# Optimization experiments

Hardware: AMD Instinct MI355X
Metric: run time of the kernel (lower is better)

The kernel has to match this reference:

```python
import jax, jax.numpy as jnp
import numpy as np
from jax import lax

B, T, S = 32, 64, 400
H, E, EMB, V = 512, 1024, 256, 32000


def setup_inputs() -> dict:
    key = jax.random.key(0)
    ks = jax.random.split(key, 16)
    w = lambda k, shape: jax.random.normal(k, shape, dtype=jnp.float32) * 0.05
    return {
        "target": jax.random.randint(ks[0], (B, T), 0, V),
        "h0": jax.random.normal(ks[1], (B, H), dtype=jnp.float32),
        "c0": jax.random.normal(ks[2], (B, H), dtype=jnp.float32),
        "enc_outs": jax.random.normal(ks[3], (S, B, E), dtype=jnp.float32),
        "attn_mask": jnp.ones((B, S), dtype=jnp.int32),
        "emb": w(ks[4], (V, EMB)),
        "W_ih": w(ks[5], (4 * H, EMB)),
        "b_ih": w(ks[6], (4 * H,)),
        "W_hh": w(ks[7], (4 * H, H)),
        "b_hh": w(ks[8], (4 * H,)),
        "W_attn": w(ks[9], (H, E)),
        "b_attn": w(ks[10], (H,)),
        "W_concat": w(ks[11], (H, E + H)),
        "b_concat": w(ks[12], (H,)),
        "W_out": w(ks[13], (V, H)),
        "b_out": w(ks[14], (V,)),
    }


def reference(target, h0, c0, enc_outs, attn_mask, emb, W_ih, b_ih, W_hh, b_hh,
              W_attn, b_attn, W_concat, b_concat, W_out, b_out):
    # Precompute attention keys projection once: [S, B, H]
    keys_proj = jnp.einsum("sbe,he->sbh", enc_outs, W_attn) + b_attn
    masked = attn_mask == 0  # [B, S]
    x_seq = emb[target].transpose(1, 0, 2)  # [T, B, EMB]

    def step(carry, x_t):
        h, c = carry
        # LSTMCell (torch gate order: i, f, g, o)
        gates = x_t @ W_ih.T + b_ih + h @ W_hh.T + b_hh  # [B, 4H]
        i, f, g, o = jnp.split(gates, 4, axis=1)
        c = jax.nn.sigmoid(f) * c + jax.nn.sigmoid(i) * jnp.tanh(g)
        h = jax.nn.sigmoid(o) * jnp.tanh(c)
        # additive-style attention: sum over hidden of query*key_proj
        scores = jnp.einsum("bh,sbh->bs", h, keys_proj)  # [B, S]
        scores = jnp.where(masked, jnp.float32(-1e18), scores)
        a = jax.nn.softmax(scores, axis=1)
        ctx = jnp.einsum("bs,sbe->be", a, enc_outs)  # [B, E]
        cat = jnp.tanh(jnp.concatenate([ctx, h], axis=1) @ W_concat.T + b_concat)
        logit = jax.nn.log_softmax(cat @ W_out.T + b_out, axis=-1)  # [B, V]
        return (h, c), logit

    (_, _), logits = lax.scan(step, (h0, c0), x_seq)  # [T, B, V]
    return logits.transpose(1, 0, 2)  # [B, T, V]
```

## Files before the change

### kernel.cpp

```cpp
#include <hip/hip_runtime.h>
#include <hip/hip_bf16.h>
#include <hip/hip_fp16.h>

#define B_ 32
#define T_ 64
#define S_ 400
#define H_ 512
#define E_ 1024
#define EMB_ 256
#define V_ 32000

typedef _Float16 f16;
typedef _Float16 half8 __attribute__((ext_vector_type(8)));
typedef float f32x4 __attribute__((ext_vector_type(4)));
typedef float f32x16 __attribute__((ext_vector_type(16)));
typedef unsigned uint4v __attribute__((ext_vector_type(4)));

__device__ __forceinline__ void gl_lds16(const void* g, void* l) {
  __builtin_amdgcn_global_load_lds(
      (const __attribute__((address_space(1))) void*)g,
      (__attribute__((address_space(3))) void*)l, 16, 0, 0);
}

__device__ __forceinline__ float sigmoidf_(float x) { return 1.f / (1.f + expf(-x)); }

__device__ __forceinline__ uint4v load_b128_sys(const void* p) {
  uint4v r;
  asm volatile("global_load_dwordx4 %0, %1, off sc0 sc1" : "=v"(r) : "v"(p) : "memory");
  return r;
}
__device__ __forceinline__ void store_b128_sys(void* p, uint4v v) {
  asm volatile("global_store_dwordx4 %0, %1, off sc0 sc1" :: "v"(p), "v"(v) : "memory");
}

__global__ __launch_bounds__(256) void cvt_f16_kernel(const float* __restrict__ src,
                                                      f16* __restrict__ dst, int n2) {
  int i = blockIdx.x * 256 + threadIdx.x;
  if (i >= n2) return;
  float2 v = reinterpret_cast<const float2*>(src)[i];
  union { f16 h[2]; unsigned u; } o;
  o.h[0] = (f16)v.x; o.h[1] = (f16)v.y;
  reinterpret_cast<unsigned*>(dst)[i] = o.u;
}

__global__ __launch_bounds__(256) void gather_x_kernel(const int* __restrict__ target,
                                                       const float* __restrict__ emb,
                                                       f16* __restrict__ xin) {
  int r = blockIdx.x;
  int t = r >> 5, b = r & 31;
  int tok = target[b * T_ + t];
  xin[(size_t)r * EMB_ + threadIdx.x] = (f16)emb[(size_t)tok * EMB_ + threadIdx.x];
}

__global__ __launch_bounds__(256) void prep_kernel(const float* __restrict__ b_ih,
                                                   const float* __restrict__ b_hh,
                                                   float* __restrict__ biasperm,
                                                   const float* __restrict__ Whh,
                                                   f16* __restrict__ Wperm,
                                                   const float* __restrict__ Wih,
                                                   f16* __restrict__ Wihp,
                                                   const float* __restrict__ h0,
                                                   f16* __restrict__ hbuf) {
  int idx = blockIdx.x * 256 + threadIdx.x;
  if (idx < 4 * H_) {
    int j = idx >> 2, gg = idx & 3;
    biasperm[idx] = b_ih[gg * H_ + j] + b_hh[gg * H_ + j];
  }
  if (idx < B_ * H_) hbuf[idx] = (f16)h0[idx];
  if (idx < T_ * B_ * H_ / 8) {
    uint4v p = {0xFFFFFFFFu, 0xFFFFFFFFu, 0xFFFFFFFFu, 0xFFFFFFFFu};
    reinterpret_cast<uint4v*>(reinterpret_cast<char*>(hbuf) + (size_t)B_ * H_ * 2)[idx] = p;
  }
  {
    int j = idx >> 9, k = idx & 511;
#pragma unroll
    for (int gg = 0; gg < 4; ++gg)
      Wperm[((size_t)(j * 4 + gg)) * H_ + k] = (f16)Whh[((size_t)(gg * H_ + j)) * H_ + k];
  }
  if (idx < H_ * EMB_) {
    int j = idx >> 8, k = idx & 255;
#pragma unroll
    for (int gg = 0; gg < 4; ++gg)
      Wihp[((size_t)(j * 4 + gg)) * EMB_ + k] = (f16)Wih[((size_t)(gg * H_ + j)) * EMB_ + k];
  }
}

template <int OUTK, bool DO_TANH>
__global__ __launch_bounds__(256) void gemm_bt_kernel(const f16* __restrict__ A,
                                                      const f16* __restrict__ W,
                                                      const float* __restrict__ bias,
                                                      void* __restrict__ outp,
                                                      int M, int N, int K) {
  __shared__ __align__(16) char As[128 * 64];
  __shared__ __align__(16) char Bs[128 * 64];
  const int tid = threadIdx.x;
  const int lane = tid & 63, wave = tid >> 6;
  const int wr = (wave >> 1) * 64, wc = (wave & 1) * 64;
  const int fr = lane & 15, fq = lane >> 4;
  const int row0 = blockIdx.x * 128, col0 = blockIdx.y * 128;

  f32x4 acc[4][4];
#pragma unroll
  for (int i = 0; i < 4; ++i)
#pragma unroll
    for (int j = 0; j < 4; ++j) acc[i][j] = {0.f, 0.f, 0.f, 0.f};

  for (int k0 = 0; k0 < K; k0 += 32) {
    __syncthreads();
#pragma unroll
    for (int i = 0; i < 2; ++i) {
      int o = tid * 16 + i * 4096;
      int r = o >> 6, kk = (o & 63) >> 1;
      gl_lds16(A + (size_t)(row0 + r) * K + (k0 + kk), As + o);
      gl_lds16(W + (size_t)(col0 + r) * K + (k0 + kk), Bs + o);
    }
    __syncthreads();
    half8 af[4], bfr[4];
#pragma unroll
    for (int mi = 0; mi < 4; ++mi)
      af[mi] = *reinterpret_cast<const half8*>(As + (wr + mi * 16 + fr) * 64 + fq * 16);
#pragma unroll
    for (int ni = 0; ni < 4; ++ni)
      bfr[ni] = *reinterpret_cast<const half8*>(Bs + (wc + ni * 16 + fr) * 64 + fq * 16);
#pragma unroll
    for (int mi = 0; mi < 4; ++mi)
#pragma unroll
      for (int ni = 0; ni < 4; ++ni)
        acc[mi][ni] = __builtin_amdgcn_mfma_f32_16x16x32_f16(af[mi], bfr[ni], acc[mi][ni], 0, 0, 0);
  }

#pragma unroll
  for (int mi = 0; mi < 4; ++mi)
#pragma unroll
    for (int ni = 0; ni < 4; ++ni)
#pragma unroll
      for (int r = 0; r < 4; ++r) {
        int row = row0 + wr + mi * 16 + fq * 4 + r;
        int col = col0 + wc + ni * 16 + fr;
        float v = acc[mi][ni][r] + bias[col];
        if (DO_TANH) v = tanhf(v);
        if (OUTK == 0) {
          ((float*)outp)[(size_t)row * N + col] = v;
        } else if (OUTK == 1) {
          ((f16*)outp)[(size_t)row * N + col] = (f16)v;
        } else {
          int orow = (row & 31) * T_ + (row >> 5);
          ((float*)outp)[(size_t)orow * N + col] = v;
        }
      }
}

__global__ __launch_bounds__(512, 1) void lstm_mfma_kernel(const float* __restrict__ xpart,
                                                           const f16* __restrict__ Wperm,
                                                           const float* __restrict__ c0,
                                                           f16* __restrict__ hbuf,
                                                           f16* __restrict__ hseq,
                                                           f16* __restrict__ catin) {
  extern __shared__ char lds[];
  char* Abuf = lds;
  float* gates = (float*)(lds + 65536);
  unsigned* hstage = (unsigned*)(lds + 65536 + 33280);
  int* flags = (int*)(lds + 65536 + 33280 + 4096);

  const int g = blockIdx.x, tid = threadIdx.x;
  const int lane = tid & 63, wave = tid >> 6;
  const int ln31 = lane & 31, lh = lane >> 5;

  if (tid < 8) flags[tid] = 0;

  half8 wf[32];
  {
    const f16* wrow = Wperm + ((size_t)(g * 256 + wave * 32 + ln31)) * H_ + lh * 8;
#pragma unroll
    for (int kc = 0; kc < 32; ++kc)
      wf[kc] = *reinterpret_cast<const half8*>(wrow + kc * 16);
  }

  const int b = tid >> 4, qd = tid & 15;
  float cst[4];
#pragma unroll
  for (int jj = 0; jj < 4; ++jj)
    cst[jj] = c0[b * H_ + g * 64 + qd * 4 + jj];

  __syncthreads();

  for (int t = 0; t < T_; ++t) {
    const float* xr = xpart + ((size_t)(t * B_ + b)) * (4 * H_) + g * 256 + qd * 16;
    float4 xv[4];
#pragma unroll
    for (int i = 0; i < 4; ++i) xv[i] = *reinterpret_cast<const float4*>(xr + i * 4);

    {
      int p = (t == 0) ? wave : (wave + (wave >= g ? 1 : 0));
      bool duty = (t == 0) ? true : (wave < 7);
      if (duty) {
        const char* sb = (const char*)hbuf + (size_t)t * 32768 + ln31 * 1024 + p * 128 + lh * 16;
        while (true) {
          uint4v v0 = load_b128_sys(sb);
          uint4v v1 = load_b128_sys(sb + 32);
          uint4v v2 = load_b128_sys(sb + 64);
          uint4v v3 = load_b128_sys(sb + 96);
          asm volatile("s_waitcnt vmcnt(0)" ::: "memory");
          __builtin_amdgcn_sched_barrier(0);
          unsigned bad = 0;
#pragma unroll
          for (int d = 0; d < 4; ++d)
            bad |= (unsigned)(v0[d] == 0xFFFFFFFFu) | (unsigned)(v1[d] == 0xFFFFFFFFu) |
                   (unsigned)(v2[d] == 0xFFFFFFFFu) | (unsigned)(v3[d] == 0xFFFFFFFFu);
          if (__all(bad == 0)) {
            char* ab = Abuf + (size_t)(t & 1) * 32768 + lane * 16;
            *(uint4v*)(ab + (size_t)(4 * p + 0) * 1024) = v0;
            *(uint4v*)(ab + (size_t)(4 * p + 1) * 1024) = v1;
            *(uint4v*)(ab + (size_t)(4 * p + 2) * 1024) = v2;
            *(uint4v*)(ab + (size_t)(4 * p + 3) * 1024) = v3;
            asm volatile("s_waitcnt lgkmcnt(0)" ::: "memory");
            __builtin_amdgcn_sched_barrier(0);
            if (lane == 0)
              __hip_atomic_fetch_add(&flags[p], 1, __ATOMIC_RELAXED,
                                     __HIP_MEMORY_SCOPE_WORKGROUP);
            break;
          }
        }
      }
    }

    f32x16 acc;
#pragma unroll
    for (int r = 0; r < 16; ++r) acc[r] = 0.f;
    const char* abR = Abuf + (size_t)(t & 1) * 32768 + lane * 16;
    const char* hsR = (const char*)hstage + lane * 16;
    const int thr = t + 1;
#pragma unroll
    for (int ps = 0; ps < 8; ++ps) {
      if (ps == g && t > 0) {
#pragma unroll
        for (int c = 0; c < 4; ++c) {
          half8 a = *(const half8*)(hsR + c * 1024);
          acc = __builtin_amdgcn_mfma_f32_32x32x16_f16(a, wf[4 * ps + c], acc, 0, 0, 0);
        }
      } else {
        while (__hip_atomic_load(&flags[ps], __ATOMIC_ACQUIRE,
                                 __HIP_MEMORY_SCOPE_WORKGROUP) < thr) {}
#pragma unroll
        for (int c = 0; c < 4; ++c) {
          half8 a = *(const half8*)(abR + (size_t)(4 * ps + c) * 1024);
          acc = __builtin_amdgcn_mfma_f32_32x32x16_f16(a, wf[4 * ps + c], acc, 0, 0, 0);
        }
      }
    }
#pragma unroll
    for (int r = 0; r < 16; ++r) {
      int row = (r & 3) + 8 * (r >> 2) + 4 * lh;
      gates[row * 260 + wave * 32 + ln31] = acc[r];
    }
    __syncthreads();

    const float* gr = &gates[b * 260 + qd * 16];
    float hv[4];
#pragma unroll
    for (int jj = 0; jj < 4; ++jj) {
      float gi = gr[jj * 4 + 0] + xv[jj].x;
      float gf = gr[jj * 4 + 1] + xv[jj].y;
      float gg = gr[jj * 4 + 2] + xv[jj].z;
      float go = gr[jj * 4 + 3] + xv[jj].w;
      cst[jj] = sigmoidf_(gf) * cst[jj] + sigmoidf_(gi) * tanhf(gg);
      hv[jj] = sigmoidf_(go) * tanhf(cst[jj]);
    }
    union { f16 h[2]; unsigned u; } pk0, pk1;
    pk0.h[0] = (f16)hv[0]; pk0.h[1] = (f16)hv[1];
    pk1.h[0] = (f16)hv[2]; pk1.h[1] = (f16)hv[3];
    {
      int cp0 = 2 * qd, cp1 = 2 * qd + 1;
      hstage[((cp0 >> 3) * 64 + ((cp0 >> 2) & 1) * 32 + b) * 4 + (cp0 & 3)] = pk0.u;
      hstage[((cp1 >> 3) * 64 + ((cp1 >> 2) & 1) * 32 + b) * 4 + (cp1 & 3)] = pk1.u;
    }
    size_t orow = (size_t)t * B_ + b;
    uint2 hpair; hpair.x = pk0.u; hpair.y = pk1.u;
    *reinterpret_cast<uint2*>(reinterpret_cast<unsigned*>(hseq) + orow * 256 + g * 32 + 2 * qd) = hpair;
    *reinterpret_cast<uint2*>(reinterpret_cast<unsigned*>(catin) + orow * 768 + 512 + g * 32 + 2 * qd) = hpair;
    __syncthreads();

    if (tid < 256) {
      int kcl = tid >> 6, l2 = tid & 63;
      uint4v v = *(const uint4v*)((const char*)hstage + (kcl * 64 + l2) * 16);
      store_b128_sys((char*)hbuf + (size_t)(t + 1) * 32768 + (l2 & 31) * 1024 +
                         g * 128 + kcl * 32 + (l2 >> 5) * 16,
                     v);
    }
  }
}

__global__ __launch_bounds__(64) void scores_kernel(const f16* __restrict__ hseq,
                                                    const f16* __restrict__ keys,
                                                    float* __restrict__ attnw) {
  int s = blockIdx.x, b = blockIdx.y;
  int t = threadIdx.x;
  const half8* hv = reinterpret_cast<const half8*>(hseq + ((size_t)t * B_ + b) * H_);
  const half8* kv = reinterpret_cast<const half8*>(keys + ((size_t)s * B_ + b) * H_);
  float acc = 0.f;
#pragma unroll 4
  for (int k = 0; k < H_ / 8; ++k) {
    half8 a = hv[k], c = kv[k];
#pragma unroll
    for (int i = 0; i < 8; ++i) acc += (float)a[i] * (float)c[i];
  }
  attnw[((size_t)b * S_ + s) * T_ + t] = acc;
}

__global__ __launch_bounds__(64) void softmax_kernel(float* __restrict__ attnw,
                                                     const int* __restrict__ mask) {
  int b = blockIdx.x, t = blockIdx.y, l = threadIdx.x;
  float vals[7];
  float m = -3.4e38f;
#pragma unroll
  for (int i = 0; i < 7; ++i) {
    int s = l + i * 64;
    float v = -3.4e38f;
    if (s < S_) {
      v = attnw[((size_t)b * S_ + s) * T_ + t];
      if (mask[b * S_ + s] == 0) v = -1e18f;
    }
    vals[i] = v;
    m = fmaxf(m, v);
  }
#pragma unroll
  for (int o = 32; o > 0; o >>= 1) m = fmaxf(m, __shfl_xor(m, o));
  float sum = 0.f;
#pragma unroll
  for (int i = 0; i < 7; ++i) {
    int s = l + i * 64;
    if (s < S_) { float e = expf(vals[i] - m); vals[i] = e; sum += e; }
  }
#pragma unroll
  for (int o = 32; o > 0; o >>= 1) sum += __shfl_xor(sum, o);
  float inv = 1.f / sum;
#pragma unroll
  for (int i = 0; i < 7; ++i) {
    int s = l + i * 64;
    if (s < S_) attnw[((size_t)b * S_ + s) * T_ + t] = vals[i] * inv;
  }
}

__global__ __launch_bounds__(256) void ctx_kernel(const float* __restrict__ attnw,
                                                  const f16* __restrict__ enc,
                                                  f16* __restrict__ catin) {
  int b = blockIdx.x, e0 = blockIdx.y * 64;
  int el = threadIdx.x & 63, tq = threadIdx.x >> 6;
  __shared__ float a_lds[100 * 64];
  float acc[16];
#pragma unroll
  for (int i = 0; i < 16; ++i) acc[i] = 0.f;
  for (int sc = 0; sc < 4; ++sc) {
    __syncthreads();
    for (int i = threadIdx.x; i < 6400; i += 256)
      a_lds[i] = attnw[((size_t)b * S_ + sc * 100) * T_ + i];
    __syncthreads();
    for (int sl = 0; sl < 100; ++sl) {
      int s = sc * 100 + sl;
      float v = (float)enc[((size_t)s * B_ + b) * E_ + e0 + el];
#pragma unroll
      for (int i = 0; i < 16; ++i) acc[i] += a_lds[sl * 64 + tq * 16 + i] * v;
    }
  }
#pragma unroll
  for (int i = 0; i < 16; ++i) {
    int t = tq * 16 + i;
    catin[((size_t)t * B_ + b) * (E_ + H_) + e0 + el] = (f16)acc[i];
  }
}

__global__ __launch_bounds__(512, 1) void logsm_kernel(float* __restrict__ out) {
  int r = blockIdx.x;
  size_t base = (size_t)r * V_;
  int tid = threadIdx.x;
  float4* op = reinterpret_cast<float4*>(out + base);
  float4 v[16];
  float m = -3.4e38f;
#pragma unroll
  for (int k = 0; k < 16; ++k) {
    int c = tid + (k << 9);
    if (c < 8000) {
      v[k] = op[c];
      m = fmaxf(m, fmaxf(fmaxf(v[k].x, v[k].y), fmaxf(v[k].z, v[k].w)));
    }
  }
  __shared__ float red[8];
#pragma unroll
  for (int o = 32; o > 0; o >>= 1) m = fmaxf(m, __shfl_xor(m, o));
  if ((tid & 63) == 0) red[tid >> 6] = m;
  __syncthreads();
  float mm = red[0];
#pragma unroll
  for (int i = 1; i < 8; ++i) mm = fmaxf(mm, red[i]);
  float s = 0.f;
#pragma unroll
  for (int k = 0; k < 16; ++k) {
    int c = tid + (k << 9);
    if (c < 8000)
      s += expf(v[k].x - mm) + expf(v[k].y - mm) + expf(v[k].z - mm) + expf(v[k].w - mm);
  }
#pragma unroll
  for (int o = 32; o > 0; o >>= 1) s += __shfl_xor(s, o);
  __syncthreads();
  if ((tid & 63) == 0) red[tid >> 6] = s;
  __syncthreads();
  s = 0.f;
#pragma unroll
  for (int i = 0; i < 8; ++i) s += red[i];
  float lse = mm + logf(s);
#pragma unroll
  for (int k = 0; k < 16; ++k) {
    int c = tid + (k << 9);
    if (c < 8000) {
      float4 o4;
      o4.x = v[k].x - lse; o4.y = v[k].y - lse;
      o4.z = v[k].z - lse; o4.w = v[k].w - lse;
      op[c] = o4;
    }
  }
}

extern "C" void kernel_launch(void* const* d_in, const int* in_sizes, int n_in,
                              void* d_out, int out_size, void* d_ws, size_t ws_size,
                              hipStream_t stream) {
  const int*   target = (const int*)d_in[0];
  const float* h0     = (const float*)d_in[1];
  const float* c0     = (const float*)d_in[2];
  const float* enc    = (const float*)d_in[3];
  const int*   mask   = (const int*)d_in[4];
  const float* emb    = (const float*)d_in[5];
  const float* W_ih   = (const float*)d_in[6];
  const float* b_ih   = (const float*)d_in[7];
  const float* W_hh   = (const float*)d_in[8];
  const float* b_hh   = (const float*)d_in[9];
  const float* W_attn = (const float*)d_in[10];
  const float* b_attn = (const float*)d_in[11];
  const float* W_cat  = (const float*)d_in[12];
  const float* b_cat  = (const float*)d_in[13];
  const float* W_out  = (const float*)d_in[14];
  const float* b_out  = (const float*)d_in[15];

  char* ws = (char*)d_ws;
  size_t off = 0;
  auto alloc = [&](size_t bytes) {
    void* p = ws + off;
    off = (off + bytes + 255) & ~(size_t)255;
    return p;
  };
  f16*   enc_f    = (f16*)alloc((size_t)S_ * B_ * E_ * 2);
  f16*   keys_f   = (f16*)alloc((size_t)S_ * B_ * H_ * 2);
  f16*   Wattn_f  = (f16*)alloc((size_t)H_ * E_ * 2);
  f16*   Wcat_f   = (f16*)alloc((size_t)H_ * (E_ + H_) * 2);
  f16*   Wout_f   = (f16*)alloc((size_t)V_ * H_ * 2);
  f16*   Wperm    = (f16*)alloc((size_t)4 * H_ * H_ * 2);
  f16*   Wihp     = (f16*)alloc((size_t)4 * H_ * EMB_ * 2);
  float* biasperm = (float*)alloc((size_t)4 * H_ * 4);
  f16*   xin_f    = (f16*)alloc((size_t)T_ * B_ * EMB_ * 2);
  float* xpart    = (float*)alloc((size_t)T_ * B_ * 4 * H_ * 4);
  f16*   hseq_f   = (f16*)alloc((size_t)T_ * B_ * H_ * 2);
  f16*   catin_f  = (f16*)alloc((size_t)T_ * B_ * (E_ + H_) * 2);
  float* attnw    = (float*)alloc((size_t)B_ * S_ * T_ * 4);
  f16*   catbuf_f = (f16*)alloc((size_t)T_ * B_ * H_ * 2);
  f16*   hbuf     = (f16*)alloc((size_t)(T_ + 1) * B_ * H_ * 2);
  (void)ws_size; (void)in_sizes; (void)n_in; (void)out_size;

  auto cvt = [&](const float* s, f16* d, size_t n) {
    int n2 = (int)(n / 2);
    cvt_f16_kernel<<<(n2 + 255) / 256, 256, 0, stream>>>(s, d, n2);
  };
  cvt(enc, enc_f, (size_t)S_ * B_ * E_);
  cvt(W_attn, Wattn_f, (size_t)H_ * E_);
  cvt(W_cat, Wcat_f, (size_t)H_ * (E_ + H_));
  cvt(W_out, Wout_f, (size_t)V_ * H_);
  gather_x_kernel<<<T_ * B_, 256, 0, stream>>>(target, emb, xin_f);
  prep_kernel<<<(H_ * H_) / 256, 256, 0, stream>>>(b_ih, b_hh, biasperm, W_hh, Wperm,
                                                   W_ih, Wihp, h0, hbuf);

  gemm_bt_kernel<1, false><<<dim3((S_ * B_) / 128, H_ / 128), 256, 0, stream>>>(
      enc_f, Wattn_f, b_attn, keys_f, S_ * B_, H_, E_);
  gemm_bt_kernel<0, false><<<dim3((T_ * B_) / 128, (4 * H_) / 128), 256, 0, stream>>>(
      xin_f, Wihp, biasperm, xpart, T_ * B_, 4 * H_, EMB_);

  lstm_mfma_kernel<<<8, 512, 65536 + 33280 + 4096 + 32, stream>>>(
      xpart, Wperm, c0, hbuf, hseq_f, catin_f);

  scores_kernel<<<dim3(S_, B_), 64, 0, stream>>>(hseq_f, keys_f, attnw);
  softmax_kernel<<<dim3(B_, T_), 64, 0, stream>>>(attnw, mask);
  ctx_kernel<<<dim3(B_, E_ / 64), 256, 0, stream>>>(attnw, enc_f, catin_f);

  gemm_bt_kernel<1, true><<<dim3((T_ * B_) / 128, H_ / 128), 256, 0, stream>>>(
      catin_f, Wcat_f, b_cat, catbuf_f, T_ * B_, H_, E_ + H_);
  gemm_bt_kernel<2, false><<<dim3((T_ * B_) / 128, V_ / 128), 256, 0, stream>>>(
      catbuf_f, Wout_f, b_out, (float*)d_out, T_ * B_, V_, H_);

  logsm_kernel<<<B_ * T_, 512, 0, stream>>>((float*)d_out);
}
```

Baseline: 876.4 us.

## Do LSTM gate math in MFMA registers and drop a per-step barrier

The recurrent LSTM kernel no longer routes MFMA accumulators through an LDS gates buffer. Lanes swap values with xor-shuffles so each lane holds the i/f/g/o gates for its own hidden columns and computes the cell update directly. The h staging buffer is double-buffered, which removes one __syncthreads per timestep. The MFMA chain is split into two accumulators for more instruction-level parallelism, and the flag increment becomes a release store. This targets the serial per-step latency of the 64-step recurrence, at the cost of shuffle overhead and scattered f16 LDS writes.

Result: no change. 887.4 us (+1.3%).

```diff
diff --git a/kernel.cpp b/kernel.cpp
--- a/kernel.cpp
+++ b/kernel.cpp
@@ -156,15 +156,14 @@
                                                            f16* __restrict__ hbuf,
                                                            f16* __restrict__ hseq,
                                                            f16* __restrict__ catin) {
-  extern __shared__ char lds[];
-  char* Abuf = lds;
-  float* gates = (float*)(lds + 65536);
-  unsigned* hstage = (unsigned*)(lds + 65536 + 33280);
-  int* flags = (int*)(lds + 65536 + 33280 + 4096);
+  __shared__ __align__(16) char Abuf[2][32768];
+  __shared__ __align__(16) f16 hstage[2][32][88];
+  __shared__ int flags[8];
 
   const int g = blockIdx.x, tid = threadIdx.x;
   const int lane = tid & 63, wave = tid >> 6;
   const int ln31 = lane & 31, lh = lane >> 5;
+  const int qq = ln31 & 3, jj = ln31 >> 2;
 
   if (tid < 8) flags[tid] = 0;
 
@@ -176,23 +175,26 @@
       wf[kc] = *reinterpret_cast<const half8*>(wrow + kc * 16);
   }
 
-  const int b = tid >> 4, qd = tid & 15;
+  const int hcol = g * 64 + wave * 8 + jj;
   float cst[4];
 #pragma unroll
-  for (int jj = 0; jj < 4; ++jj)
-    cst[jj] = c0[b * H_ + g * 64 + qd * 4 + jj];
+  for (int rg = 0; rg < 4; ++rg)
+    cst[rg] = c0[(qq + 8 * rg + 4 * lh) * H_ + hcol];
 
   __syncthreads();
 
   for (int t = 0; t < T_; ++t) {
-    const float* xr = xpart + ((size_t)(t * B_ + b)) * (4 * H_) + g * 256 + qd * 16;
     float4 xv[4];
-#pragma unroll
-    for (int i = 0; i < 4; ++i) xv[i] = *reinterpret_cast<const float4*>(xr + i * 4);
+    {
+      const float* xb = xpart + ((size_t)t * B_) * 2048 + g * 256 + wave * 32 + 4 * jj;
+#pragma unroll
+      for (int rg = 0; rg < 4; ++rg)
+        xv[rg] = *reinterpret_cast<const float4*>(xb + (size_t)(qq + 8 * rg + 4 * lh) * 2048);
+    }
 
     {
       int p = (t == 0) ? wave : (wave + (wave >= g ? 1 : 0));
-      bool duty = (t == 0) ? true : (wave < 7);
+      bool duty = (t == 0) || (wave < 7);
       if (duty) {
         const char* sb = (const char*)hbuf + (size_t)t * 32768 + ln31 * 1024 + p * 128 + lh * 16;
         while (true) {
@@ -208,7 +210,7 @@
             bad |= (unsigned)(v0[d] == 0xFFFFFFFFu) | (unsigned)(v1[d] == 0xFFFFFFFFu) |
                    (unsigned)(v2[d] == 0xFFFFFFFFu) | (unsigned)(v3[d] == 0xFFFFFFFFu);
           if (__all(bad == 0)) {
-            char* ab = Abuf + (size_t)(t & 1) * 32768 + lane * 16;
+            char* ab = Abuf[t & 1] + lane * 16;
             *(uint4v*)(ab + (size_t)(4 * p + 0) * 1024) = v0;
             *(uint4v*)(ab + (size_t)(4 * p + 1) * 1024) = v1;
             *(uint4v*)(ab + (size_t)(4 * p + 2) * 1024) = v2;
@@ -216,76 +218,84 @@
             asm volatile("s_waitcnt lgkmcnt(0)" ::: "memory");
             __builtin_amdgcn_sched_barrier(0);
             if (lane == 0)
-              __hip_atomic_fetch_add(&flags[p], 1, __ATOMIC_RELAXED,
-                                     __HIP_MEMORY_SCOPE_WORKGROUP);
+              __hip_atomic_store(&flags[p], t + 1, __ATOMIC_RELEASE,
+                                 __HIP_MEMORY_SCOPE_WORKGROUP);
             break;
           }
         }
       }
     }
 
-    f32x16 acc;
-#pragma unroll
-    for (int r = 0; r < 16; ++r) acc[r] = 0.f;
-    const char* abR = Abuf + (size_t)(t & 1) * 32768 + lane * 16;
-    const char* hsR = (const char*)hstage + lane * 16;
-    const int thr = t + 1;
+    f32x16 acA, acB;
+#pragma unroll
+    for (int r = 0; r < 16; ++r) { acA[r] = 0.f; acB[r] = 0.f; }
+    const char* abR = Abuf[t & 1] + lane * 16;
+    const f16* hsR = &hstage[(t + 1) & 1][ln31][0];
 #pragma unroll
     for (int ps = 0; ps < 8; ++ps) {
+      half8 a[4];
       if (ps == g && t > 0) {
 #pragma unroll
-        for (int c = 0; c < 4; ++c) {
-          half8 a = *(const half8*)(hsR + c * 1024);
-          acc = __builtin_amdgcn_mfma_f32_32x32x16_f16(a, wf[4 * ps + c], acc, 0, 0, 0);
-        }
+        for (int c = 0; c < 4; ++c)
+          a[c] = *reinterpret_cast<const half8*>(hsR + c * 16 + lh * 8);
       } else {
         while (__hip_atomic_load(&flags[ps], __ATOMIC_ACQUIRE,
-                                 __HIP_MEMORY_SCOPE_WORKGROUP) < thr) {}
-#pragma unroll
-        for (int c = 0; c < 4; ++c) {
-          half8 a = *(const half8*)(abR + (size_t)(4 * ps + c) * 1024);
-          acc = __builtin_amdgcn_mfma_f32_32x32x16_f16(a, wf[4 * ps + c], acc, 0, 0, 0);
-        }
+                                 __HIP_MEMORY_SCOPE_WORKGROUP) < t + 1) {}
+#pragma unroll
+        for (int c = 0; c < 4; ++c)
+          a[c] = *reinterpret_cast<const half8*>(abR + (size_t)(4 * ps + c) * 1024);
       }
-    }
-#pragma unroll
-    for (int r = 0; r < 16; ++r) {
-      int row = (r & 3) + 8 * (r >> 2) + 4 * lh;
-      gates[row * 260 + wave * 32 + ln31] = acc[r];
+      if (ps & 1) {
+#pragma unroll
+        for (int c = 0; c < 4; ++c)
+          acB = __builtin_amdgcn_mfma_f32_32x32x16_f16(a[c], wf[4 * ps + c], acB, 0, 0, 0);
+      } else {
+#pragma unroll
+        for (int c = 0; c < 4; ++c)
+          acA = __builtin_amdgcn_mfma_f32_32x32x16_f16(a[c], wf[4 * ps + c], acA, 0, 0, 0);
+      }
+    }
+    f32x16 acc = acA + acB;
+
+    float u[16];
+#pragma unroll
+    for (int rg = 0; rg < 4; ++rg) {
+      float a0 = acc[rg * 4 + 0], a1 = acc[rg * 4 + 1];
+      float a2 = acc[rg * 4 + 2], a3 = acc[rg * 4 + 3];
+      bool o1 = (qq & 1) != 0;
+      float t01 = o1 ? a0 : a1; float r01 = __shfl_xor(t01, 1);
+      a0 = o1 ? r01 : a0;  a1 = o1 ? a1 : r01;
+      float t23 = o1 ? a2 : a3; float r23 = __shfl_xor(t23, 1);
+      a2 = o1 ? r23 : a2;  a3 = o1 ? a3 : r23;
+      bool o2 = (qq & 2) != 0;
+      float t02 = o2 ? a0 : a2; float r02 = __shfl_xor(t02, 2);
+      a0 = o2 ? r02 : a0;  a2 = o2 ? a2 : r02;
+      float t13 = o2 ? a1 : a3; float r13 = __shfl_xor(t13, 2);
+      a1 = o2 ? r13 : a1;  a3 = o2 ? a3 : r13;
+      u[rg * 4 + 0] = a0; u[rg * 4 + 1] = a1; u[rg * 4 + 2] = a2; u[rg * 4 + 3] = a3;
+    }
+
+#pragma unroll
+    for (int rg = 0; rg < 4; ++rg) {
+      float gi = u[rg * 4 + 0] + xv[rg].x;
+      float gf = u[rg * 4 + 1] + xv[rg].y;
+      float gg = u[rg * 4 + 2] + xv[rg].z;
+      float go = u[rg * 4 + 3] + xv[rg].w;
+      float c2 = sigmoidf_(gf) * cst[rg] + sigmoidf_(gi) * tanhf(gg);
+      cst[rg] = c2;
+      float h = sigmoidf_(go) * tanhf(c2);
+      hstage[t & 1][qq + 8 * rg + 4 * lh][wave * 8 + jj] = (f16)h;
     }
     __syncthreads();
 
-    const float* gr = &gates[b * 260 + qd * 16];
-    float hv[4];
-#pragma unroll
-    for (int jj = 0; jj < 4; ++jj) {
-      float gi = gr[jj * 4 + 0] + xv[jj].x;
-      float gf = gr[jj * 4 + 1] + xv[jj].y;
-      float gg = gr[jj * 4 + 2] + xv[jj].z;
-      float go = gr[jj * 4 + 3] + xv[jj].w;
-      cst[jj] = sigmoidf_(gf) * cst[jj] + sigmoidf_(gi) * tanhf(gg);
-      hv[jj] = sigmoidf_(go) * tanhf(cst[jj]);
-    }
-    union { f16 h[2]; unsigned u; } pk0, pk1;
-    pk0.h[0] = (f16)hv[0]; pk0.h[1] = (f16)hv[1];
-    pk1.h[0] = (f16)hv[2]; pk1.h[1] = (f16)hv[3];
-    {
-      int cp0 = 2 * qd, cp1 = 2 * qd + 1;
-      hstage[((cp0 >> 3) * 64 + ((cp0 >> 2) & 1) * 32 + b) * 4 + (cp0 & 3)] = pk0.u;
-      hstage[((cp1 >> 3) * 64 + ((cp1 >> 2) & 1) * 32 + b) * 4 + (cp1 & 3)] = pk1.u;
-    }
-    size_t orow = (size_t)t * B_ + b;
-    uint2 hpair; hpair.x = pk0.u; hpair.y = pk1.u;
-    *reinterpret_cast<uint2*>(reinterpret_cast<unsigned*>(hseq) + orow * 256 + g * 32 + 2 * qd) = hpair;
-    *reinterpret_cast<uint2*>(reinterpret_cast<unsigned*>(catin) + orow * 768 + 512 + g * 32 + 2 * qd) = hpair;
-    __syncthreads();
-
     if (tid < 256) {
-      int kcl = tid >> 6, l2 = tid & 63;
-      uint4v v = *(const uint4v*)((const char*)hstage + (kcl * 64 + l2) * 16);
-      store_b128_sys((char*)hbuf + (size_t)(t + 1) * 32768 + (l2 & 31) * 1024 +
-                         g * 128 + kcl * 32 + (l2 >> 5) * 16,
+      int b = tid >> 3, c8 = tid & 7;
+      uint4v v = *reinterpret_cast<const uint4v*>(&hstage[t & 1][b][c8 * 8]);
+      store_b128_sys((char*)hbuf + (size_t)(t + 1) * 32768 + b * 1024 + g * 128 +
+                         (c8 >> 1) * 32 + (c8 & 1) * 16,
                      v);
+      *(uint4v*)((char*)hseq + ((size_t)t * B_ + b) * 1024 + g * 128 + c8 * 16) = v;
+      *(uint4v*)((char*)catin + ((size_t)t * B_ + b) * 3072 + 2048 + g * 128 + c8 * 16) = v;
     }
   }
 }
@@ -481,8 +491,7 @@
   gemm_bt_kernel<0, false><<<dim3((T_ * B_) / 128, (4 * H_) / 128), 256, 0, stream>>>(
       xin_f, Wihp, biasperm, xpart, T_ * B_, 4 * H_, EMB_);
 
-  lstm_mfma_kernel<<<8, 512, 65536 + 33280 + 4096 + 32, stream>>>(
-      xpart, Wperm, c0, hbuf, hseq_f, catin_f);
+  lstm_mfma_kernel<<<8, 512, 0, stream>>>(xpart, Wperm, c0, hbuf, hseq_f, catin_f);
 
   scores_kernel<<<dim3(S_, B_), 64, 0, stream>>>(hseq_f, keys_f, attnw);
   softmax_kernel<<<dim3(B_, T_), 64, 0, stream>>>(attnw, mask);
```

## Use MFMA for attention scores, reuse hbuf as hseq, fuse conversions

Applied to the files above, without the earlier changes.

Replaces the scalar per-(s,b) dot-product scores kernel with an MFMA kernel that computes 32x64 tiles of key–query products per wave. The key buffer is padded to 512 rows, and results for rows beyond S are discarded. The LSTM kernel no longer writes separate hseq and catin copies; the recurrent hbuf buffer is reused as hseq, and a small copy kernel fills the h half of the concat input. The four fp32-to-fp16 conversion launches are merged into one kernel, trading launch overhead for per-thread branching.

Measured after the change: 791.0 us. -9.7%, faster.

```diff
diff --git a/kernel.cpp b/kernel.cpp
--- a/kernel.cpp
+++ b/kernel.cpp
@@ -5,6 +5,7 @@
 #define B_ 32
 #define T_ 64
 #define S_ 400
+#define SPAD_ 512
 #define H_ 512
 #define E_ 1024
 #define EMB_ 256
@@ -33,14 +34,30 @@
   asm volatile("global_store_dwordx4 %0, %1, off sc0 sc1" :: "v"(p), "v"(v) : "memory");
 }
 
-__global__ __launch_bounds__(256) void cvt_f16_kernel(const float* __restrict__ src,
-                                                      f16* __restrict__ dst, int n2) {
+#define N2_ENC (S_ * B_ * E_ / 2)
+#define N2_WA  (H_ * E_ / 2)
+#define N2_WC  (H_ * (E_ + H_) / 2)
+#define N2_WO  (V_ * H_ / 2)
+#define N2_TOT (N2_ENC + N2_WA + N2_WC + N2_WO)
+__global__ __launch_bounds__(256) void cvt_all_kernel(const float* __restrict__ enc,
+                                                      const float* __restrict__ wa,
+                                                      const float* __restrict__ wc,
+                                                      const float* __restrict__ wo,
+                                                      f16* __restrict__ enc_f,
+                                                      f16* __restrict__ wa_f,
+                                                      f16* __restrict__ wc_f,
+                                                      f16* __restrict__ wo_f) {
   int i = blockIdx.x * 256 + threadIdx.x;
-  if (i >= n2) return;
-  float2 v = reinterpret_cast<const float2*>(src)[i];
+  if (i >= N2_TOT) return;
+  const float* s; f16* d; int j;
+  if (i < N2_ENC) { s = enc; d = enc_f; j = i; }
+  else if (i < N2_ENC + N2_WA) { s = wa; d = wa_f; j = i - N2_ENC; }
+  else if (i < N2_ENC + N2_WA + N2_WC) { s = wc; d = wc_f; j = i - N2_ENC - N2_WA; }
+  else { s = wo; d = wo_f; j = i - N2_ENC - N2_WA - N2_WC; }
+  float2 v = reinterpret_cast<const float2*>(s)[j];
   union { f16 h[2]; unsigned u; } o;
   o.h[0] = (f16)v.x; o.h[1] = (f16)v.y;
-  reinterpret_cast<unsigned*>(dst)[i] = o.u;
+  reinterpret_cast<unsigned*>(d)[j] = o.u;
 }
 
 __global__ __launch_bounds__(256) void gather_x_kernel(const int* __restrict__ target,
@@ -153,9 +170,7 @@
 __global__ __launch_bounds__(512, 1) void lstm_mfma_kernel(const float* __restrict__ xpart,
                                                            const f16* __restrict__ Wperm,
                                                            const float* __restrict__ c0,
-                                                           f16* __restrict__ hbuf,
-                                                           f16* __restrict__ hseq,
-                                                           f16* __restrict__ catin) {
+                                                           f16* __restrict__ hbuf) {
   extern __shared__ char lds[];
   char* Abuf = lds;
   float* gates = (float*)(lds + 65536);
@@ -274,10 +289,6 @@
       hstage[((cp0 >> 3) * 64 + ((cp0 >> 2) & 1) * 32 + b) * 4 + (cp0 & 3)] = pk0.u;
       hstage[((cp1 >> 3) * 64 + ((cp1 >> 2) & 1) * 32 + b) * 4 + (cp1 & 3)] = pk1.u;
     }
-    size_t orow = (size_t)t * B_ + b;
-    uint2 hpair; hpair.x = pk0.u; hpair.y = pk1.u;
-    *reinterpret_cast<uint2*>(reinterpret_cast<unsigned*>(hseq) + orow * 256 + g * 32 + 2 * qd) = hpair;
-    *reinterpret_cast<uint2*>(reinterpret_cast<unsigned*>(catin) + orow * 768 + 512 + g * 32 + 2 * qd) = hpair;
     __syncthreads();
 
     if (tid < 256) {
@@ -290,21 +301,43 @@
   }
 }
 
-__global__ __launch_bounds__(64) void scores_kernel(const f16* __restrict__ hseq,
-                                                    const f16* __restrict__ keys,
-                                                    float* __restrict__ attnw) {
-  int s = blockIdx.x, b = blockIdx.y;
-  int t = threadIdx.x;
-  const half8* hv = reinterpret_cast<const half8*>(hseq + ((size_t)t * B_ + b) * H_);
-  const half8* kv = reinterpret_cast<const half8*>(keys + ((size_t)s * B_ + b) * H_);
-  float acc = 0.f;
-#pragma unroll 4
-  for (int k = 0; k < H_ / 8; ++k) {
-    half8 a = hv[k], c = kv[k];
-#pragma unroll
-    for (int i = 0; i < 8; ++i) acc += (float)a[i] * (float)c[i];
-  }
-  attnw[((size_t)b * S_ + s) * T_ + t] = acc;
+__global__ __launch_bounds__(128) void catcopy_kernel(const f16* __restrict__ hseq,
+                                                      f16* __restrict__ catin) {
+  int r = blockIdx.x;
+  const uint2* src = reinterpret_cast<const uint2*>(hseq + (size_t)r * H_);
+  uint2* dst = reinterpret_cast<uint2*>(catin + (size_t)r * (E_ + H_) + E_);
+  dst[threadIdx.x] = src[threadIdx.x];
+}
+
+__global__ __launch_bounds__(256) void scores_mfma_kernel(const f16* __restrict__ keys,
+                                                          const f16* __restrict__ hseq,
+                                                          float* __restrict__ attnw) {
+  const int b = blockIdx.y;
+  const int lane = threadIdx.x & 63, wave = threadIdx.x >> 6;
+  const int ln31 = lane & 31, lh = lane >> 5;
+  const int stile = blockIdx.x * 128 + wave * 32;
+  const f16* ar  = keys + ((size_t)(stile + ln31) * B_ + b) * H_ + lh * 8;
+  const f16* br0 = hseq + ((size_t)ln31 * B_ + b) * H_ + lh * 8;
+  const f16* br1 = hseq + ((size_t)(ln31 + 32) * B_ + b) * H_ + lh * 8;
+  f32x16 ac0, ac1;
+#pragma unroll
+  for (int r = 0; r < 16; ++r) { ac0[r] = 0.f; ac1[r] = 0.f; }
+#pragma unroll
+  for (int kc = 0; kc < 32; ++kc) {
+    half8 a  = *reinterpret_cast<const half8*>(ar + kc * 16);
+    half8 h0 = *reinterpret_cast<const half8*>(br0 + kc * 16);
+    half8 h1 = *reinterpret_cast<const half8*>(br1 + kc * 16);
+    ac0 = __builtin_amdgcn_mfma_f32_32x32x16_f16(a, h0, ac0, 0, 0, 0);
+    ac1 = __builtin_amdgcn_mfma_f32_32x32x16_f16(a, h1, ac1, 0, 0, 0);
+  }
+#pragma unroll
+  for (int r = 0; r < 16; ++r) {
+    int s = stile + (r & 3) + 8 * (r >> 2) + 4 * lh;
+    if (s < S_) {
+      attnw[((size_t)b * S_ + s) * T_ + ln31]      = ac0[r];
+      attnw[((size_t)b * S_ + s) * T_ + 32 + ln31] = ac1[r];
+    }
+  }
 }
 
 __global__ __launch_bounds__(64) void softmax_kernel(float* __restrict__ attnw,
@@ -448,7 +481,7 @@
     return p;
   };
   f16*   enc_f    = (f16*)alloc((size_t)S_ * B_ * E_ * 2);
-  f16*   keys_f   = (f16*)alloc((size_t)S_ * B_ * H_ * 2);
+  f16*   keys_f   = (f16*)alloc((size_t)SPAD_ * B_ * H_ * 2);
   f16*   Wattn_f  = (f16*)alloc((size_t)H_ * E_ * 2);
   f16*   Wcat_f   = (f16*)alloc((size_t)H_ * (E_ + H_) * 2);
   f16*   Wout_f   = (f16*)alloc((size_t)V_ * H_ * 2);
@@ -457,21 +490,16 @@
   float* biasperm = (float*)alloc((size_t)4 * H_ * 4);
   f16*   xin_f    = (f16*)alloc((size_t)T_ * B_ * EMB_ * 2);
   float* xpart    = (float*)alloc((size_t)T_ * B_ * 4 * H_ * 4);
-  f16*   hseq_f   = (f16*)alloc((size_t)T_ * B_ * H_ * 2);
   f16*   catin_f  = (f16*)alloc((size_t)T_ * B_ * (E_ + H_) * 2);
   float* attnw    = (float*)alloc((size_t)B_ * S_ * T_ * 4);
   f16*   catbuf_f = (f16*)alloc((size_t)T_ * B_ * H_ * 2);
   f16*   hbuf     = (f16*)alloc((size_t)(T_ + 1) * B_ * H_ * 2);
   (void)ws_size; (void)in_sizes; (void)n_in; (void)out_size;
 
-  auto cvt = [&](const float* s, f16* d, size_t n) {
-    int n2 = (int)(n / 2);
-    cvt_f16_kernel<<<(n2 + 255) / 256, 256, 0, stream>>>(s, d, n2);
-  };
-  cvt(enc, enc_f, (size_t)S_ * B_ * E_);
-  cvt(W_attn, Wattn_f, (size_t)H_ * E_);
-  cvt(W_cat, Wcat_f, (size_t)H_ * (E_ + H_));
-  cvt(W_out, Wout_f, (size_t)V_ * H_);
+  f16* hseq_f = hbuf + (size_t)B_ * H_;
+
+  cvt_all_kernel<<<(N2_TOT + 255) / 256, 256, 0, stream>>>(
+      enc, W_attn, W_cat, W_out, enc_f, Wattn_f, Wcat_f, Wout_f);
   gather_x_kernel<<<T_ * B_, 256, 0, stream>>>(target, emb, xin_f);
   prep_kernel<<<(H_ * H_) / 256, 256, 0, stream>>>(b_ih, b_hh, biasperm, W_hh, Wperm,
                                                    W_ih, Wihp, h0, hbuf);
@@ -481,10 +509,10 @@
   gemm_bt_kernel<0, false><<<dim3((T_ * B_) / 128, (4 * H_) / 128), 256, 0, stream>>>(
       xin_f, Wihp, biasperm, xpart, T_ * B_, 4 * H_, EMB_);
 
-  lstm_mfma_kernel<<<8, 512, 65536 + 33280 + 4096 + 32, stream>>>(
-      xpart, Wperm, c0, hbuf, hseq_f, catin_f);
-
-  scores_kernel<<<dim3(S_, B_), 64, 0, stream>>>(hseq_f, keys_f, attnw);
+  lstm_mfma_kernel<<<8, 512, 65536 + 33280 + 4096 + 32, stream>>>(xpart, Wperm, c0, hbuf);
+
+  catcopy_kernel<<<T_ * B_, 128, 0, stream>>>(hseq_f, catin_f);
+  scores_mfma_kernel<<<dim3(SPAD_ / 128, B_), 256, 0, stream>>>(keys_f, hseq_f, attnw);
   softmax_kernel<<<dim3(B_, T_), 64, 0, stream>>>(attnw, mask);
   ctx_kernel<<<dim3(B_, E_ / 64), 256, 0, stream>>>(attnw, enc_f, catin_f);
 
```
